# Performance work log

Measured on AMD Instinct MI355X. Metric: run time of the kernel, lower is better.

## Reference

```python
import jax, jax.numpy as jnp
import numpy as np

V, B, P = 32, 128, 256   # views/directions, batch, max points per diagram
J = 75                   # n_elements (structure elements)
NF = 32                  # n_filters (= directions)
S2 = 25                  # stage_2_out
NU = 0.1
BN_EPS = 1e-5


def _transform(births, lifetimes):
    """UpperDiagonalThresholdedLogTransform(nu=0.1) on (birth, death) points."""
    deaths = births + lifetimes + 0.01
    inv = jnp.asarray(1.0 / np.sqrt(2.0), births.dtype)
    x = (births + deaths) * inv          # rotated 1st coord
    y = (deaths - births) * inv          # rotated 2nd coord (persistence), > 0
    y = jnp.where(y <= NU, jnp.log(y / NU) * NU + NU, y)
    return jnp.stack([x, y], axis=-1)    # [V,B,P,2]


def _batchnorm(x, gamma, beta, axis):
    mean = x.mean(axis=axis, keepdims=True)
    var = x.var(axis=axis, keepdims=True)  # biased, training-mode BN
    return (x - mean) / jnp.sqrt(var + BN_EPS) * gamma + beta


def setup_inputs() -> dict:
    key = jax.random.key(0)
    ks = jax.random.split(key, 20)
    inp = {
        "births": jax.random.uniform(ks[0], (V, B, P), jnp.float32),
        "lifetimes": jax.random.uniform(ks[1], (V, B, P), jnp.float32),
        "mask": jax.random.randint(ks[2], (V, B, P), 0, 2).astype(jnp.int32),
        # SLayerPHT params (one SLayer per view)
        "centers": jax.random.uniform(ks[3], (V, J, 2), jnp.float32),
        "sharpness": 4.0 + 0.1 * jax.random.normal(ks[4], (V, J, 2), jnp.float32),
        # stage_1: Conv1d(3->NF, k=1, no bias), Conv1d(NF->8, k=1, no bias)
        "w1": 0.1 * jax.random.normal(ks[5], (V, NF, 3), jnp.float32),
        "w2": 0.1 * jax.random.normal(ks[6], (V, 8, NF), jnp.float32),
        # stage_2: Linear(J->S2), BN(S2), Linear(S2->S2)
        "l1_w": 0.1 * jax.random.normal(ks[7], (V, S2, J), jnp.float32),
        "l1_b": 0.1 * jax.random.normal(ks[8], (V, S2), jnp.float32),
        "bn1_g": jnp.ones((V, S2), jnp.float32),
        "bn1_b": jnp.zeros((V, S2), jnp.float32),
        "l2_w": 0.1 * jax.random.normal(ks[9], (V, S2, S2), jnp.float32),
        "l2_b": 0.1 * jax.random.normal(ks[10], (V, S2), jnp.float32),
        # linear_1: Linear(V*S2 -> 500) + BN(500); linear_2: Linear(500 -> 200)
        "fc1_w": 0.05 * jax.random.normal(ks[11], (500, V * S2), jnp.float32),
        "fc1_b": 0.05 * jax.random.normal(ks[12], (500,), jnp.float32),
        "bn2_g": jnp.ones((500,), jnp.float32),
        "bn2_b": jnp.zeros((500,), jnp.float32),
        "fc2_w": 0.05 * jax.random.normal(ks[13], (200, 500), jnp.float32),
        "fc2_b": 0.05 * jax.random.normal(ks[14], (200,), jnp.float32),
    }
    return inp


def reference(births, lifetimes, mask, centers, sharpness, w1, w2,
              l1_w, l1_b, bn1_g, bn1_b, l2_w, l2_b,
              fc1_w, fc1_b, bn2_g, bn2_b, fc2_w, fc2_b):
    q = _transform(births, lifetimes)                 # [V,B,P,2]
    m = mask.astype(q.dtype)                          # [V,B,P]
    # SLayer: z[v,b,j] = sum_p m * exp(-sum_d s[v,j,d]^2 (q[v,b,p,d]-c[v,j,d])^2)
    s2 = sharpness * sharpness                        # [V,J,2]
    qa = jnp.concatenate([q * q, q, jnp.ones_like(q[..., :1])], axis=-1)  # [V,B,P,5]
    ca = jnp.concatenate([s2, -2.0 * s2 * centers,
                          (s2 * centers * centers).sum(-1, keepdims=True)], axis=-1)  # [V,J,5]
    d2 = jnp.einsum('vbpk,vjk->vbpj', qa, ca)         # squared weighted distance
    z = jnp.einsum('vbpj,vbp->vbj', jnp.exp(-d2), m)  # [V,B,J]
    # neighbor-direction stacking (n_neighbor_directions=1, cyclic): [i-1, i, i+1]
    zn = jnp.stack([jnp.roll(z, 1, axis=0), z, jnp.roll(z, -1, axis=0)], axis=2)  # [V,B,3,J]
    # stage_1: two 1x1 conv1d (no bias), then max over channels
    h = jnp.einsum('vbcj,vfc->vbfj', zn, w1)          # [V,B,NF,J]
    h = jnp.einsum('vbfj,vgf->vbgj', h, w2)           # [V,B,8,J]
    h = h.max(axis=2)                                 # [V,B,J]
    # stage_2: Linear -> BN(train) -> Linear -> ReLU (Dropout = eval identity)
    u = jnp.einsum('vbj,voj->vbo', h, l1_w) + l1_b[:, None, :]   # [V,B,S2]
    u = _batchnorm(u, bn1_g[:, None, :], bn1_b[:, None, :], axis=1)
    u = jnp.einsum('vbo,vpo->vbp', u, l2_w) + l2_b[:, None, :]
    u = jax.nn.relu(u)
    x = u.transpose(1, 0, 2).reshape(B, V * S2)       # torch.cat(x, 1)
    x = x @ fc1_w.T + fc1_b
    x = _batchnorm(x, bn2_g, bn2_b, axis=0)
    x = x @ fc2_w.T + fc2_b                           # [B,200]
    return x
```

## Files before the change

kernel.cpp:

```cpp
#include <hip/hip_runtime.h>

#define V 32
#define B 128
#define P 256
#define J 75
#define NF 32
#define S2 25

__global__ __launch_bounds__(256) void slayer_kernel(
    const float* __restrict__ births,
    const float* __restrict__ lifetimes,
    const int* __restrict__ mask,
    const float* __restrict__ centers,
    const float* __restrict__ sharpness,
    float* __restrict__ z)
{
    const int vb = blockIdx.x;
    const int v  = vb >> 7;
    const int tid = threadIdx.x;
    const int lane = tid & 63;

    __shared__ float4 pts[P];
    __shared__ int cnt;
    __shared__ float part[2][J];

    if (tid == 0) cnt = 0;
    __syncthreads();

    const float inv = 0.70710678118654752f;
    {
        const int gi = vb * P + tid;
        float b0 = births[gi];
        float l0 = lifetimes[gi];
        int   m  = mask[gi];
        float d  = b0 + l0 + 0.01f;
        float x  = (b0 + d) * inv;
        float y  = (d - b0) * inv;
        if (y <= 0.1f) y = __logf(y * 10.0f) * 0.1f + 0.1f;

        bool keep = (m != 0);
        unsigned long long bal = __ballot(keep);
        unsigned long long lt  = (1ull << lane) - 1ull;
        int prefix = __popcll(bal & lt);
        int total  = __popcll(bal);
        int base = 0;
        if (lane == 0) base = atomicAdd(&cnt, total);
        base = __shfl(base, 0, 64);
        if (keep) pts[base + prefix] = make_float4(x, y, x * x, y * y);
    }
    __syncthreads();

    const int n = cnt;
    float acc = 0.f;
    if (tid < 3 * J) {
        const int pid = tid / J;
        const int j   = tid - pid * J;
        const int cj  = (v * J + j) * 2;
        float cx = centers[cj + 0];
        float cy = centers[cj + 1];
        float sx = sharpness[cj + 0];
        float sy = sharpness[cj + 1];
        float s2x = sx * sx, s2y = sy * sy;
        float k0 = -s2x;
        float k1 = -s2y;
        float k2 = 2.0f * s2x * cx;
        float k3 = 2.0f * s2y * cy;
        float kc = -(s2x * cx * cx + s2y * cy * cy);
        const int p0 = (n * pid) / 3;
        const int p1 = (n * (pid + 1)) / 3;
        #pragma unroll 4
        for (int p = p0; p < p1; ++p) {
            float4 a = pts[p];
            float d = fmaf(k0, a.z, kc);
            d = fmaf(k1, a.w, d);
            d = fmaf(k2, a.x, d);
            d = fmaf(k3, a.y, d);
            acc += __expf(d);
        }
        if (pid > 0) part[pid - 1][j] = acc;
    }
    __syncthreads();

    if (tid < J)
        z[vb * J + tid] = acc + part[0][tid] + part[1][tid];
}

__global__ __launch_bounds__(1024) void stage2_kernel(
    const float* __restrict__ z,
    const float* __restrict__ w1,
    const float* __restrict__ w2,
    const float* __restrict__ l1_w,
    const float* __restrict__ l1_b,
    const float* __restrict__ bn1_g,
    const float* __restrict__ bn1_b,
    const float* __restrict__ l2_w,
    const float* __restrict__ l2_b,
    float* __restrict__ xT)
{
    const int v   = blockIdx.x;
    const int tid = threadIdx.x;
    const int vm  = (v + V - 1) & (V - 1);
    const int vp  = (v + 1) & (V - 1);

    __shared__ float wcomb[8][3];
    __shared__ float l1ws[S2 * J];
    __shared__ float l1bs[S2];
    __shared__ float wl2[S2 * S2];
    __shared__ float l2bs[S2];
    __shared__ float hs[B * J];
    __shared__ float us[B * S2];
    __shared__ float sred[32 * S2], ssred[32 * S2];
    __shared__ float sc[S2], sh[S2];

    if (tid < 24) {
        int g = tid / 3, c = tid - g * 3;
        const float* w2r = w2 + v * 8 * NF + g * NF;
        const float* w1c = w1 + v * NF * 3 + c;
        float s = 0.f;
        #pragma unroll
        for (int f = 0; f < NF; ++f) s += w2r[f] * w1c[f * 3];
        wcomb[g][c] = s;
    }
    for (int i = tid; i < S2 * J;  i += 1024) l1ws[i] = l1_w[v * S2 * J + i];
    for (int i = tid; i < S2 * S2; i += 1024) wl2[i]  = l2_w[v * S2 * S2 + i];
    if (tid < S2) { l1bs[tid] = l1_b[v * S2 + tid]; l2bs[tid] = l2_b[v * S2 + tid]; }
    __syncthreads();

    for (int t = tid; t < B * J; t += 1024) {
        float a0 = z[vm * (B * J) + t];
        float a1 = z[v  * (B * J) + t];
        float a2 = z[vp * (B * J) + t];
        float hm = -3.4e38f;
        #pragma unroll
        for (int g = 0; g < 8; ++g) {
            float s = wcomb[g][0] * a0 + wcomb[g][1] * a1 + wcomb[g][2] * a2;
            hm = fmaxf(hm, s);
        }
        hs[t] = hm;
    }
    __syncthreads();

    for (int t = tid; t < S2 * B; t += 1024) {
        int o = t >> 7;
        int b = t & 127;
        float acc = l1bs[o];
        const float* hrow = hs + b * J;
        const float* wrow = l1ws + o * J;
        #pragma unroll 5
        for (int j = 0; j < J; ++j) acc += hrow[j] * wrow[j];
        us[b * S2 + o] = acc;
    }
    __syncthreads();

    if (tid < 32 * S2) {
        int c = tid / S2;
        int o = tid - c * S2;
        float s = 0.f, ss = 0.f;
        #pragma unroll
        for (int b = c * 4; b < c * 4 + 4; ++b) {
            float x = us[b * S2 + o];
            s += x; ss += x * x;
        }
        sred[tid] = s; ssred[tid] = ss;
    }
    __syncthreads();

    if (tid < S2) {
        float s = 0.f, ss = 0.f;
        #pragma unroll
        for (int c = 0; c < 32; ++c) { s += sred[c * S2 + tid]; ss += ssred[c * S2 + tid]; }
        float mean = s * (1.f / B);
        float var  = ss * (1.f / B) - mean * mean;
        float istd = rsqrtf(var + 1e-5f);
        float g  = bn1_g[v * S2 + tid];
        float be = bn1_b[v * S2 + tid];
        sc[tid] = g * istd;
        sh[tid] = be - mean * g * istd;
    }
    __syncthreads();

    for (int i = tid; i < B * S2; i += 1024) {
        int o = i % S2;
        us[i] = us[i] * sc[o] + sh[o];
    }
    __syncthreads();

    for (int t = tid; t < S2 * B; t += 1024) {
        int p = t >> 7;
        int b = t & 127;
        float acc = l2bs[p];
        const float* urow = us + b * S2;
        const float* wrow = wl2 + p * S2;
        #pragma unroll
        for (int o = 0; o < S2; ++o) acc += urow[o] * wrow[o];
        acc = fmaxf(acc, 0.f);
        xT[(v * S2 + p) * B + b] = acc;
    }
}

__global__ __launch_bounds__(256) void fc1_bn2_kernel(
    const float* __restrict__ xT,
    const float* __restrict__ fc1_w,
    const float* __restrict__ fc1_b,
    const float* __restrict__ bn2_g,
    const float* __restrict__ bn2_b,
    float* __restrict__ y1n)
{
    const int n  = blockIdx.x;
    const int tid = threadIdx.x;
    const int kk = tid >> 7;
    const int b  = tid & 127;
    const int K  = V * S2;

    __shared__ float wsm[V * S2];
    __shared__ float pr[B];
    __shared__ float red[2][2];

    for (int i = tid; i < K; i += 256) wsm[i] = fc1_w[n * K + i];
    __syncthreads();

    float acc = 0.f;
    const float* xp = xT + kk * 400 * B + b;
    const float* wp = wsm + kk * 400;
    for (int k = 0; k < 400; ++k) acc += xp[k * B] * wp[k];

    if (kk == 1) pr[b] = acc;
    __syncthreads();

    float t = 0.f;
    if (kk == 0) {
        t = acc + pr[b] + fc1_b[n];
        const int wave = tid >> 6;
        const int lane = tid & 63;
        float s = t, ss = t * t;
        #pragma unroll
        for (int off = 32; off > 0; off >>= 1) {
            s  += __shfl_down(s,  off, 64);
            ss += __shfl_down(ss, off, 64);
        }
        if (lane == 0) { red[wave][0] = s; red[wave][1] = ss; }
    }
    __syncthreads();

    if (kk == 0) {
        float s  = red[0][0] + red[1][0];
        float ss = red[0][1] + red[1][1];
        float mean = s * (1.f / B);
        float var  = ss * (1.f / B) - mean * mean;
        float istd = rsqrtf(var + 1e-5f);
        float g   = bn2_g[n];
        float be  = bn2_b[n];
        float scl = g * istd;
        y1n[n * B + b] = t * scl + (be - mean * scl);
    }
}

__global__ __launch_bounds__(256) void fc2_kernel(
    const float* __restrict__ y1n,
    const float* __restrict__ fc2_w,
    const float* __restrict__ fc2_b,
    float* __restrict__ out)
{
    const int n2 = blockIdx.x;
    const int tid = threadIdx.x;
    const int kk = tid >> 7;
    const int b  = tid & 127;

    __shared__ float wsm[500];
    __shared__ float pr[B];
    for (int i = tid; i < 500; i += 256) wsm[i] = fc2_w[n2 * 500 + i];
    __syncthreads();

    float acc = 0.f;
    const float* yp = y1n + kk * 250 * B + b;
    const float* wp = wsm + kk * 250;
    for (int k = 0; k < 250; ++k) acc += yp[k * B] * wp[k];

    if (kk == 1) pr[b] = acc;
    __syncthreads();

    if (kk == 0)
        out[b * 200 + n2] = acc + pr[b] + fc2_b[n2];
}

extern "C" void kernel_launch(void* const* d_in, const int* in_sizes, int n_in,
                              void* d_out, int out_size, void* d_ws, size_t ws_size,
                              hipStream_t stream) {
    const float* births    = (const float*)d_in[0];
    const float* lifetimes = (const float*)d_in[1];
    const int*   mask      = (const int*)d_in[2];
    const float* centers   = (const float*)d_in[3];
    const float* sharpness = (const float*)d_in[4];
    const float* w1        = (const float*)d_in[5];
    const float* w2        = (const float*)d_in[6];
    const float* l1_w      = (const float*)d_in[7];
    const float* l1_b      = (const float*)d_in[8];
    const float* bn1_g     = (const float*)d_in[9];
    const float* bn1_b     = (const float*)d_in[10];
    const float* l2_w      = (const float*)d_in[11];
    const float* l2_b      = (const float*)d_in[12];
    const float* fc1_w     = (const float*)d_in[13];
    const float* fc1_b     = (const float*)d_in[14];
    const float* bn2_g     = (const float*)d_in[15];
    const float* bn2_b     = (const float*)d_in[16];
    const float* fc2_w     = (const float*)d_in[17];
    const float* fc2_b     = (const float*)d_in[18];
    float* out = (float*)d_out;

    float* ws    = (float*)d_ws;
    float* z     = ws;
    float* xT    = ws + 307200;
    float* y1n   = ws + 307200 + 102400;

    slayer_kernel <<<V * B, 256, 0, stream>>>(births, lifetimes, mask, centers, sharpness, z);
    stage2_kernel <<<V, 1024, 0, stream>>>(z, w1, w2, l1_w, l1_b, bn1_g, bn1_b,
                                           l2_w, l2_b, xT);
    fc1_bn2_kernel<<<500, 256, 0, stream>>>(xT, fc1_w, fc1_b, bn2_g, bn2_b, y1n);
    fc2_kernel    <<<200, 256, 0, stream>>>(y1n, fc2_w, fc2_b, out);
}
```

Baseline: 147.8 us.

## Fuse fc1 into stage2 via atomics, merge bn2 with fc2, retile slayer

The slayer kernel now splits the points eight ways per (view, batch) block, and each thread evaluates three structure-element centers per loaded point. It also zeroes the fc1 accumulator buffer. Stage2 keeps its per-view activations in shared memory and multiplies them by that view's slice of fc1_w. It accumulates the fc1 output with global float atomics, which removes the xT round trip and a separate fc1 launch. A single kernel then computes the bn2 statistics and the fc2 output, two output columns per block. In exchange, stage2 uses much more LDS, there is atomic contention across 32 view blocks, and the float summation order becomes non-deterministic.

```diff
diff --git a/kernel.cpp b/kernel.cpp
--- a/kernel.cpp
+++ b/kernel.cpp
@@ -6,6 +6,7 @@
 #define J 75
 #define NF 32
 #define S2 25
+#define N1 500
 
 __global__ __launch_bounds__(256) void slayer_kernel(
     const float* __restrict__ births,
@@ -13,16 +14,22 @@
     const int* __restrict__ mask,
     const float* __restrict__ centers,
     const float* __restrict__ sharpness,
-    float* __restrict__ z)
+    float* __restrict__ z,
+    float* __restrict__ acc_out)
 {
     const int vb = blockIdx.x;
     const int v  = vb >> 7;
     const int tid = threadIdx.x;
     const int lane = tid & 63;
 
+    {
+        const int base = vb * 16;
+        if (tid < 16 && base + tid < N1 * B) acc_out[base + tid] = 0.f;
+    }
+
     __shared__ float4 pts[P];
     __shared__ int cnt;
-    __shared__ float part[2][J];
+    __shared__ float part[8 * J];
 
     if (tid == 0) cnt = 0;
     __syncthreads();
@@ -51,38 +58,53 @@
     __syncthreads();
 
     const int n = cnt;
-    float acc = 0.f;
-    if (tid < 3 * J) {
-        const int pid = tid / J;
-        const int j   = tid - pid * J;
-        const int cj  = (v * J + j) * 2;
-        float cx = centers[cj + 0];
-        float cy = centers[cj + 1];
-        float sx = sharpness[cj + 0];
-        float sy = sharpness[cj + 1];
-        float s2x = sx * sx, s2y = sy * sy;
-        float k0 = -s2x;
-        float k1 = -s2y;
-        float k2 = 2.0f * s2x * cx;
-        float k3 = 2.0f * s2y * cy;
-        float kc = -(s2x * cx * cx + s2y * cy * cy);
-        const int p0 = (n * pid) / 3;
-        const int p1 = (n * (pid + 1)) / 3;
-        #pragma unroll 4
+    const int pid = tid >> 5;
+    const int t32 = tid & 31;
+    if (t32 < 25) {
+        const int j0 = t32 * 3;
+        float k0[3], k1[3], k2[3], k3[3], kc[3];
+        #pragma unroll
+        for (int c = 0; c < 3; ++c) {
+            const int cj = (v * J + j0 + c) * 2;
+            float cx = centers[cj + 0];
+            float cy = centers[cj + 1];
+            float sx = sharpness[cj + 0];
+            float sy = sharpness[cj + 1];
+            float s2x = sx * sx, s2y = sy * sy;
+            k0[c] = -s2x;
+            k1[c] = -s2y;
+            k2[c] = 2.0f * s2x * cx;
+            k3[c] = 2.0f * s2y * cy;
+            kc[c] = -(s2x * cx * cx + s2y * cy * cy);
+        }
+        float a0 = 0.f, a1 = 0.f, a2 = 0.f;
+        const int p0 = (n * pid) >> 3;
+        const int p1 = (n * (pid + 1)) >> 3;
+        #pragma unroll 2
         for (int p = p0; p < p1; ++p) {
             float4 a = pts[p];
-            float d = fmaf(k0, a.z, kc);
-            d = fmaf(k1, a.w, d);
-            d = fmaf(k2, a.x, d);
-            d = fmaf(k3, a.y, d);
-            acc += __expf(d);
-        }
-        if (pid > 0) part[pid - 1][j] = acc;
-    }
-    __syncthreads();
-
-    if (tid < J)
-        z[vb * J + tid] = acc + part[0][tid] + part[1][tid];
+            float d0 = fmaf(k0[0], a.z, kc[0]);
+            d0 = fmaf(k1[0], a.w, d0); d0 = fmaf(k2[0], a.x, d0); d0 = fmaf(k3[0], a.y, d0);
+            float d1 = fmaf(k0[1], a.z, kc[1]);
+            d1 = fmaf(k1[1], a.w, d1); d1 = fmaf(k2[1], a.x, d1); d1 = fmaf(k3[1], a.y, d1);
+            float d2 = fmaf(k0[2], a.z, kc[2]);
+            d2 = fmaf(k1[2], a.w, d2); d2 = fmaf(k2[2], a.x, d2); d2 = fmaf(k3[2], a.y, d2);
+            a0 += __expf(d0);
+            a1 += __expf(d1);
+            a2 += __expf(d2);
+        }
+        part[pid * J + j0 + 0] = a0;
+        part[pid * J + j0 + 1] = a1;
+        part[pid * J + j0 + 2] = a2;
+    }
+    __syncthreads();
+
+    if (tid < J) {
+        float s = 0.f;
+        #pragma unroll
+        for (int q = 0; q < 8; ++q) s += part[q * J + tid];
+        z[vb * J + tid] = s;
+    }
 }
 
 __global__ __launch_bounds__(1024) void stage2_kernel(
@@ -95,7 +117,8 @@
     const float* __restrict__ bn1_b,
     const float* __restrict__ l2_w,
     const float* __restrict__ l2_b,
-    float* __restrict__ xT)
+    const float* __restrict__ fc1_w,
+    float* __restrict__ acc_out)
 {
     const int v   = blockIdx.x;
     const int tid = threadIdx.x;
@@ -109,6 +132,8 @@
     __shared__ float l2bs[S2];
     __shared__ float hs[B * J];
     __shared__ float us[B * S2];
+    __shared__ float xs[S2 * B];
+    __shared__ float fw[N1 * S2];
     __shared__ float sred[32 * S2], ssred[32 * S2];
     __shared__ float sc[S2], sh[S2];
 
@@ -123,6 +148,10 @@
     }
     for (int i = tid; i < S2 * J;  i += 1024) l1ws[i] = l1_w[v * S2 * J + i];
     for (int i = tid; i < S2 * S2; i += 1024) wl2[i]  = l2_w[v * S2 * S2 + i];
+    for (int i = tid; i < N1 * S2; i += 1024) {
+        int nn = i / S2, p = i - nn * S2;
+        fw[i] = fc1_w[nn * (V * S2) + v * S2 + p];
+    }
     if (tid < S2) { l1bs[tid] = l1_b[v * S2 + tid]; l2bs[tid] = l2_b[v * S2 + tid]; }
     __syncthreads();
 
@@ -193,94 +222,90 @@
         const float* wrow = wl2 + p * S2;
         #pragma unroll
         for (int o = 0; o < S2; ++o) acc += urow[o] * wrow[o];
-        acc = fmaxf(acc, 0.f);
-        xT[(v * S2 + p) * B + b] = acc;
+        xs[p * B + b] = fmaxf(acc, 0.f);
+    }
+    __syncthreads();
+
+    for (int t = tid; t < N1 * B; t += 1024) {
+        int nn = t >> 7;
+        int b  = t & 127;
+        const float* fr = fw + nn * S2;
+        const float* xc = xs + b;
+        float s = 0.f;
+        #pragma unroll
+        for (int p = 0; p < S2; ++p) s += fr[p] * xc[p * B];
+        atomicAdd(&acc_out[nn * B + b], s);
     }
 }
 
-__global__ __launch_bounds__(256) void fc1_bn2_kernel(
-    const float* __restrict__ xT,
-    const float* __restrict__ fc1_w,
+__global__ __launch_bounds__(256) void bn2_fc2_kernel(
+    const float* __restrict__ acc_in,
     const float* __restrict__ fc1_b,
     const float* __restrict__ bn2_g,
     const float* __restrict__ bn2_b,
-    float* __restrict__ y1n)
-{
-    const int n  = blockIdx.x;
-    const int tid = threadIdx.x;
-    const int kk = tid >> 7;
-    const int b  = tid & 127;
-    const int K  = V * S2;
-
-    __shared__ float wsm[V * S2];
-    __shared__ float pr[B];
-    __shared__ float red[2][2];
-
-    for (int i = tid; i < K; i += 256) wsm[i] = fc1_w[n * K + i];
-    __syncthreads();
-
-    float acc = 0.f;
-    const float* xp = xT + kk * 400 * B + b;
-    const float* wp = wsm + kk * 400;
-    for (int k = 0; k < 400; ++k) acc += xp[k * B] * wp[k];
-
-    if (kk == 1) pr[b] = acc;
-    __syncthreads();
-
-    float t = 0.f;
-    if (kk == 0) {
-        t = acc + pr[b] + fc1_b[n];
-        const int wave = tid >> 6;
-        const int lane = tid & 63;
-        float s = t, ss = t * t;
-        #pragma unroll
-        for (int off = 32; off > 0; off >>= 1) {
-            s  += __shfl_down(s,  off, 64);
-            ss += __shfl_down(ss, off, 64);
-        }
-        if (lane == 0) { red[wave][0] = s; red[wave][1] = ss; }
-    }
-    __syncthreads();
-
-    if (kk == 0) {
-        float s  = red[0][0] + red[1][0];
-        float ss = red[0][1] + red[1][1];
-        float mean = s * (1.f / B);
-        float var  = ss * (1.f / B) - mean * mean;
-        float istd = rsqrtf(var + 1e-5f);
-        float g   = bn2_g[n];
-        float be  = bn2_b[n];
-        float scl = g * istd;
-        y1n[n * B + b] = t * scl + (be - mean * scl);
-    }
-}
-
-__global__ __launch_bounds__(256) void fc2_kernel(
-    const float* __restrict__ y1n,
     const float* __restrict__ fc2_w,
     const float* __restrict__ fc2_b,
     float* __restrict__ out)
 {
-    const int n2 = blockIdx.x;
+    const int k0  = blockIdx.x * 2;
     const int tid = threadIdx.x;
+
+    __shared__ float w0s[N1], w1s[N1];
+    __shared__ float fbs[N1];
+    __shared__ float sred[2 * N1], ssred[2 * N1];
+    __shared__ float scl[N1], shs[N1];
+    __shared__ float pr0[B], pr1[B];
+
+    for (int i = tid; i < N1; i += 256) {
+        w0s[i] = fc2_w[k0 * N1 + i];
+        w1s[i] = fc2_w[(k0 + 1) * N1 + i];
+        fbs[i] = fc1_b[i];
+    }
+    __syncthreads();
+
+    for (int idx = tid; idx < 2 * N1; idx += 256) {
+        int nn = idx >> 1;
+        int c  = idx & 1;
+        const float* ap = acc_in + nn * B + c * 64;
+        float fb = fbs[nn];
+        float s = 0.f, ss = 0.f;
+        #pragma unroll 8
+        for (int j = 0; j < 64; ++j) {
+            float x = ap[j] + fb;
+            s += x; ss += x * x;
+        }
+        sred[idx] = s; ssred[idx] = ss;
+    }
+    __syncthreads();
+
+    for (int nn = tid; nn < N1; nn += 256) {
+        float s  = sred[2 * nn] + sred[2 * nn + 1];
+        float ss = ssred[2 * nn] + ssred[2 * nn + 1];
+        float mean = s * (1.f / B);
+        float var  = ss * (1.f / B) - mean * mean;
+        float istd = rsqrtf(var + 1e-5f);
+        float g  = bn2_g[nn];
+        float be = bn2_b[nn];
+        scl[nn] = g * istd;
+        shs[nn] = be - mean * g * istd;
+    }
+    __syncthreads();
+
     const int kk = tid >> 7;
     const int b  = tid & 127;
-
-    __shared__ float wsm[500];
-    __shared__ float pr[B];
-    for (int i = tid; i < 500; i += 256) wsm[i] = fc2_w[n2 * 500 + i];
-    __syncthreads();
-
-    float acc = 0.f;
-    const float* yp = y1n + kk * 250 * B + b;
-    const float* wp = wsm + kk * 250;
-    for (int k = 0; k < 250; ++k) acc += yp[k * B] * wp[k];
-
-    if (kk == 1) pr[b] = acc;
-    __syncthreads();
-
-    if (kk == 0)
-        out[b * 200 + n2] = acc + pr[b] + fc2_b[n2];
+    float a0 = 0.f, a1 = 0.f;
+    for (int nn = kk * 250; nn < kk * 250 + 250; ++nn) {
+        float y = (acc_in[nn * B + b] + fbs[nn]) * scl[nn] + shs[nn];
+        a0 += y * w0s[nn];
+        a1 += y * w1s[nn];
+    }
+    if (kk == 1) { pr0[b] = a0; pr1[b] = a1; }
+    __syncthreads();
+
+    if (kk == 0) {
+        out[b * 200 + k0]     = a0 + pr0[b] + fc2_b[k0];
+        out[b * 200 + k0 + 1] = a1 + pr1[b] + fc2_b[k0 + 1];
+    }
 }
 
 extern "C" void kernel_launch(void* const* d_in, const int* in_sizes, int n_in,
@@ -307,14 +332,14 @@
     const float* fc2_b     = (const float*)d_in[18];
     float* out = (float*)d_out;
 
-    float* ws    = (float*)d_ws;
-    float* z     = ws;
-    float* xT    = ws + 307200;
-    float* y1n   = ws + 307200 + 102400;
-
-    slayer_kernel <<<V * B, 256, 0, stream>>>(births, lifetimes, mask, centers, sharpness, z);
+    float* ws  = (float*)d_ws;
+    float* z   = ws;
+    float* acc = ws + 307200;
+
+    slayer_kernel <<<V * B, 256, 0, stream>>>(births, lifetimes, mask, centers,
+                                              sharpness, z, acc);
     stage2_kernel <<<V, 1024, 0, stream>>>(z, w1, w2, l1_w, l1_b, bn1_g, bn1_b,
-                                           l2_w, l2_b, xT);
-    fc1_bn2_kernel<<<500, 256, 0, stream>>>(xT, fc1_w, fc1_b, bn2_g, bn2_b, y1n);
-    fc2_kernel    <<<200, 256, 0, stream>>>(y1n, fc2_w, fc2_b, out);
+                                           l2_w, l2_b, fc1_w, acc);
+    bn2_fc2_kernel<<<100, 256, 0, stream>>>(acc, fc1_b, bn2_g, bn2_b,
+                                            fc2_w, fc2_b, out);
 }
```

New measurement: 173.0 us. 1.17x slower.
